# Kernel tuning notes

Measured on AMD Instinct MI355X. Metric: run time of the kernel, lower is better.

The kernel has to match this reference:

```python
import jax, jax.numpy as jnp
import numpy as np

B, S, D = 1, 2048, 2048
H, G, HD = 32, 8, 64        # n_heads, n_kv_groups, head_dim
GS = H // G                  # group_size
ROPE_BASE = 10000.0


def _rope_tables(seq_len, head_dim):
    inv_freq = 1.0 / (ROPE_BASE ** (jnp.arange(0, head_dim, 2, dtype=jnp.float32) / head_dim))
    angles = jnp.arange(seq_len, dtype=jnp.float32)[:, None] * inv_freq[None, :]  # [S, HD/2]
    angles = jnp.concatenate([angles, angles], axis=-1)                            # [S, HD]
    return jnp.cos(angles), jnp.sin(angles)


def setup_inputs() -> dict:
    key = jax.random.key(0)
    ks = jax.random.split(key, 5)
    x = jax.random.normal(ks[0], (B, S, D), dtype=jnp.float32)
    mask = jnp.triu(jnp.ones((S, S), dtype=bool), k=1)  # True = masked (causal)
    cos_vals, sin_vals = _rope_tables(S, HD)
    scale = 0.02
    Wq = jax.random.normal(ks[1], (H * HD, D), dtype=jnp.float32) * scale
    Wk = jax.random.normal(ks[2], (G * HD, D), dtype=jnp.float32) * scale
    Wv = jax.random.normal(ks[3], (G * HD, D), dtype=jnp.float32) * scale
    Wo = jax.random.normal(ks[4], (D, H * HD), dtype=jnp.float32) * scale
    return {"x": x, "mask": mask, "cos_vals": cos_vals, "sin_vals": sin_vals,
            "Wq": Wq, "Wk": Wk, "Wv": Wv, "Wo": Wo}


def _apply_rope(t, cos, sin):
    # t: [b, heads, S, HD]; cos/sin: [S, HD]
    half = t.shape[-1] // 2
    t1, t2 = t[..., :half], t[..., half:]
    rotated = jnp.concatenate([-t2, t1], axis=-1)
    return t * cos[None, None] + rotated * sin[None, None]


def reference(x, mask, cos_vals, sin_vals, Wq, Wk, Wv, Wo):
    b, s, _ = x.shape
    q = (x @ Wq.T).reshape(b, s, H, HD).transpose(0, 2, 1, 3)   # [b,H,S,HD]
    k = (x @ Wk.T).reshape(b, s, G, HD).transpose(0, 2, 1, 3)   # [b,G,S,HD]
    v = (x @ Wv.T).reshape(b, s, G, HD).transpose(0, 2, 1, 3)   # [b,G,S,HD]
    q = _apply_rope(q, cos_vals, sin_vals)
    k = _apply_rope(k, cos_vals, sin_vals)
    # Group-broadcast instead of repeat_interleave (same math)
    q = q.reshape(b, G, GS, s, HD)
    scores = jnp.einsum('bghqd,bgkd->bghqk', q, k)              # [b,G,GS,S,S]
    scores = jnp.where(mask[None, None, None], -jnp.inf, scores)
    weights = jax.nn.softmax(scores / np.sqrt(HD).astype(np.float32), axis=-1)
    out = jnp.einsum('bghqk,bgkd->bghqd', weights, v)           # [b,G,GS,S,HD]
    out = out.reshape(b, H, s, HD).transpose(0, 2, 1, 3).reshape(b, s, H * HD)
    return out @ Wo.T
```

## Files before the change

kernel.cpp:

```cpp
#include <hip/hip_runtime.h>
#include <cstddef>
#include <cstdint>

#define S 2048
#define Dm 2048
#define NH 32
#define NG 8
#define HD 64

typedef __attribute__((ext_vector_type(8))) short bf16x8;
typedef __attribute__((ext_vector_type(4))) short bf16x4;
typedef __attribute__((ext_vector_type(4))) float f32x4;

__device__ __forceinline__ float fast_exp2(float x) { return __builtin_amdgcn_exp2f(x); }

__device__ __forceinline__ unsigned short f2bf(float f) {
  unsigned int u = __builtin_bit_cast(unsigned int, f);
  u = (u + 0x7fffu + ((u >> 16) & 1u)) >> 16;
  return (unsigned short)u;
}
__device__ __forceinline__ unsigned int pk2bf(float lo, float hi) {
  unsigned int a = __builtin_bit_cast(unsigned int, lo) + 0x8000u;
  unsigned int b = __builtin_bit_cast(unsigned int, hi) + 0x8000u;
  return (a >> 16) | (b & 0xffff0000u);
}
__device__ __forceinline__ void gl_lds16(const unsigned short* g, unsigned short* l) {
  __builtin_amdgcn_global_load_lds(
      (const __attribute__((address_space(1))) unsigned int*)g,
      (__attribute__((address_space(3))) unsigned int*)l, 16, 0, 0);
}

#define QSC 0.1803368801111601f

__global__ __launch_bounds__(256) void cvt_all(const float* __restrict__ x,
                                               const float* __restrict__ Wq,
                                               const float* __restrict__ Wk,
                                               const float* __restrict__ Wv,
                                               const float* __restrict__ Wo,
                                               unsigned short* __restrict__ xb,
                                               unsigned short* __restrict__ Wcat,
                                               unsigned short* __restrict__ Wob) {
  int i = blockIdx.x * 256 + threadIdx.x;
  const float4* src;
  ushort4* dst;
  if (i < 1048576)      { src = (const float4*)x  + i;             dst = (ushort4*)xb + i; }
  else if (i < 2097152) { src = (const float4*)Wq + (i - 1048576); dst = (ushort4*)Wcat + (i - 1048576); }
  else if (i < 2359296) { src = (const float4*)Wk + (i - 2097152); dst = (ushort4*)Wcat + 1048576 + (i - 2097152); }
  else if (i < 2621440) { src = (const float4*)Wv + (i - 2359296); dst = (ushort4*)Wcat + 1310720 + (i - 2359296); }
  else                  { src = (const float4*)Wo + (i - 2621440); dst = (ushort4*)Wob + (i - 2621440); }
  float4 v = *src;
  ushort4 o;
  o.x = f2bf(v.x); o.y = f2bf(v.y); o.z = f2bf(v.z); o.w = f2bf(v.w);
  *dst = o;
}

__global__ __launch_bounds__(256) void gemm_bf16(const unsigned short* __restrict__ A,
                                                 const unsigned short* __restrict__ B,
                                                 float* __restrict__ Cf,
                                                 unsigned short* __restrict__ Cb,
                                                 unsigned short* __restrict__ VtOut,
                                                 const float* __restrict__ cosv,
                                                 const float* __restrict__ sinv,
                                                 int M, int N, int K) {
  __shared__ __align__(16) unsigned short As[64 * 64];
  __shared__ __align__(16) unsigned short Bs[128 * 64];
  const int tid = threadIdx.x;
  const int lane = tid & 63, wave = tid >> 6;
  const int row0 = blockIdx.y * 64, col0 = blockIdx.x * 128;
  const int wr = (wave >> 1) * 32, wc = (wave & 1) * 64;

  f32x4 acc[2][4];
#pragma unroll
  for (int i = 0; i < 2; i++)
#pragma unroll
    for (int j = 0; j < 4; j++) acc[i][j] = (f32x4){0.f, 0.f, 0.f, 0.f};

  const int arow0 = tid >> 3, aslot0 = ((tid & 7) ^ (arow0 & 7)) * 8;
  const int arow1 = (tid + 256) >> 3, aslot1 = (((tid + 256) & 7) ^ (arow1 & 7)) * 8;
  const int fr = lane & 15, q4 = lane >> 4;

  for (int k0 = 0; k0 < K; k0 += 64) {
    gl_lds16(&A[(size_t)(row0 + arow0) * K + k0 + aslot0], &As[tid * 8]);
    gl_lds16(&A[(size_t)(row0 + arow1) * K + k0 + aslot1], &As[(tid + 256) * 8]);
#pragma unroll
    for (int b = 0; b < 4; b++) {
      int p = tid + b * 256;
      int r = p >> 3, sl = ((p & 7) ^ (r & 7)) * 8;
      gl_lds16(&B[(size_t)(col0 + r) * K + k0 + sl], &Bs[p * 8]);
    }
    __syncthreads();
#pragma unroll
    for (int kk = 0; kk < 2; kk++) {
      bf16x8 af[2], bfr[4];
#pragma unroll
      for (int i = 0; i < 2; i++) {
        int R = wr + i * 16 + fr;
        af[i] = *(const bf16x8*)&As[R * 64 + ((q4 + kk * 4) ^ (R & 7)) * 8];
      }
#pragma unroll
      for (int j = 0; j < 4; j++) {
        int R = wc + j * 16 + fr;
        bfr[j] = *(const bf16x8*)&Bs[R * 64 + ((q4 + kk * 4) ^ (R & 7)) * 8];
      }
#pragma unroll
      for (int i = 0; i < 2; i++)
#pragma unroll
        for (int j = 0; j < 4; j++)
          acc[i][j] = __builtin_amdgcn_mfma_f32_16x16x32_bf16(af[i], bfr[j], acc[i][j], 0, 0, 0);
    }
    __syncthreads();
  }

  const int cc = lane & 15, cr = (lane >> 4) * 4;

  if (cosv) {
#pragma unroll
    for (int i = 0; i < 2; i++) {
      int grb = row0 + wr + i * 16 + cr;
#pragma unroll
      for (int j = 0; j < 2; j++) {
        int gc = col0 + wc + j * 16 + cc;
        if (gc < 2560) {
          int d = j * 16 + cc;
          float qs = (gc < 2048) ? QSC : 1.0f;
#pragma unroll
          for (int r = 0; r < 4; r++) {
            float c = cosv[(grb + r) * 64 + d];
            float s = sinv[(grb + r) * 64 + d];
            float t1 = acc[i][j][r], t2 = acc[i][j + 2][r];
            acc[i][j][r]     = (t1 * c - t2 * s) * qs;
            acc[i][j + 2][r] = (t2 * c + t1 * s) * qs;
          }
        }
      }
    }
  }

#pragma unroll
  for (int i = 0; i < 2; i++)
#pragma unroll
    for (int j = 0; j < 4; j++) {
      int gc = col0 + wc + j * 16 + cc;
#pragma unroll
      for (int r = 0; r < 4; r++) {
        int gr = row0 + wr + i * 16 + cr + r;
        if (cosv) {
          if (gc >= 2560) VtOut[(size_t)(gc - 2560) * 2048 + gr] = f2bf(acc[i][j][r]);
          else            Cb[(size_t)gr * N + gc] = f2bf(acc[i][j][r]);
        } else if (Cf)    Cf[(size_t)gr * N + gc] = acc[i][j][r];
        else              Cb[(size_t)gr * N + gc] = f2bf(acc[i][j][r]);
      }
    }
}

__global__ __launch_bounds__(256, 2) void flash_mfma(const unsigned short* __restrict__ QKV,
                                                     const unsigned short* __restrict__ Vt_g,
                                                     unsigned short* __restrict__ Ob) {
  __shared__ __align__(16) unsigned short Ks[2][64 * 64];
  __shared__ __align__(16) unsigned short Vs[2][64 * 64];

  const int tid = threadIdx.x;
  const int lane = tid & 63, wave = tid >> 6;
  const int m15 = lane & 15, q4 = lane >> 4;

  const int L = blockIdx.x;
  const int h = L & 31, g = h >> 2;
  const int u0 = L >> 5, a = u0 >> 3, b = u0 & 7;
  const int u = (a == 0) ? 15 - b : b;
  const int qb = u * 128;
  const int ntiles = 2 * u + 2;

  bf16x8 qf[2][2];
#pragma unroll
  for (int f = 0; f < 2; f++) {
    const size_t qrow = (size_t)(qb + f * 64 + wave * 16 + m15) * 3072 + h * 64;
    qf[f][0] = *(const bf16x8*)&QKV[qrow + q4 * 8];
    qf[f][1] = *(const bf16x8*)&QKV[qrow + 32 + q4 * 8];
  }

  f32x4 accO[2][4];
  float l_lane[2] = {0.f, 0.f};
#pragma unroll
  for (int f = 0; f < 2; f++)
#pragma unroll
    for (int v = 0; v < 4; v++) accO[f][v] = (f32x4){0.f, 0.f, 0.f, 0.f};

  const int p0 = wave * 128 + lane, p1 = p0 + 64;
  const int sr0 = p0 >> 3, so0 = ((p0 & 7) ^ (sr0 & 7)) * 8;
  const int sr1 = p1 >> 3, so1 = ((p1 & 7) ^ (sr1 & 7)) * 8;

#pragma unroll
  for (int t = 0; t < 2; t++) {
    const int k0 = t * 64;
    gl_lds16(&QKV[(size_t)(k0 + sr0) * 3072 + 2048 + g * 64 + so0], &Ks[t][p0 * 8]);
    gl_lds16(&QKV[(size_t)(k0 + sr1) * 3072 + 2048 + g * 64 + so1], &Ks[t][p1 * 8]);
    gl_lds16(&Vt_g[(size_t)(g * 64 + sr0) * 2048 + k0 + so0], &Vs[t][p0 * 8]);
    gl_lds16(&Vt_g[(size_t)(g * 64 + sr1) * 2048 + k0 + so1], &Vs[t][p1 * 8]);
  }

  for (int t = 0; t < ntiles; t++) {
    if (t + 1 < ntiles) asm volatile("s_waitcnt vmcnt(4)" ::: "memory");
    else                asm volatile("s_waitcnt vmcnt(0)" ::: "memory");
    asm volatile("s_barrier" ::: "memory");

    const unsigned short* Kb = Ks[t & 1];
    const unsigned short* Vb = Vs[t & 1];
    const bool act0 = (t < ntiles - 1);

    f32x4 sc[2][4];
#pragma unroll
    for (int kt = 0; kt < 4; kt++) {
      const int krow = kt * 16 + m15;
      bf16x8 kf0 = *(const bf16x8*)&Kb[krow * 64 + (q4 ^ (krow & 7)) * 8];
      bf16x8 kf1 = *(const bf16x8*)&Kb[krow * 64 + ((q4 + 4) ^ (krow & 7)) * 8];
      f32x4 z1 = (f32x4){0.f, 0.f, 0.f, 0.f};
      z1 = __builtin_amdgcn_mfma_f32_16x16x32_bf16(kf0, qf[1][0], z1, 0, 0, 0);
      sc[1][kt] = __builtin_amdgcn_mfma_f32_16x16x32_bf16(kf1, qf[1][1], z1, 0, 0, 0);
      if (act0) {
        f32x4 z0 = (f32x4){0.f, 0.f, 0.f, 0.f};
        z0 = __builtin_amdgcn_mfma_f32_16x16x32_bf16(kf0, qf[0][0], z0, 0, 0, 0);
        sc[0][kt] = __builtin_amdgcn_mfma_f32_16x16x32_bf16(kf1, qf[0][1], z0, 0, 0, 0);
      }
    }

    bf16x8 pA0[2], pA1[2];
#pragma unroll
    for (int f = 0; f < 2; f++) {
      if (f == 0 && !act0) continue;
      if (t == 2 * u + f) {
        const int qo = wave * 16 + m15;
#pragma unroll
        for (int kt = 0; kt < 4; kt++)
#pragma unroll
          for (int r = 0; r < 4; r++)
            if (kt * 16 + q4 * 4 + r > qo) sc[f][kt][r] = -1e30f;
      }
      float rs = 0.f;
#pragma unroll
      for (int kt = 0; kt < 4; kt++)
#pragma unroll
        for (int r = 0; r < 4; r++) {
          float p = fast_exp2(sc[f][kt][r]);
          sc[f][kt][r] = p;
          rs += p;
        }
      l_lane[f] += rs;

      int4 pa0, pa1;
      pa0.x = pk2bf(sc[f][0][0], sc[f][0][1]); pa0.y = pk2bf(sc[f][0][2], sc[f][0][3]);
      pa0.z = pk2bf(sc[f][1][0], sc[f][1][1]); pa0.w = pk2bf(sc[f][1][2], sc[f][1][3]);
      pa1.x = pk2bf(sc[f][2][0], sc[f][2][1]); pa1.y = pk2bf(sc[f][2][2], sc[f][2][3]);
      pa1.z = pk2bf(sc[f][3][0], sc[f][3][1]); pa1.w = pk2bf(sc[f][3][2], sc[f][3][3]);
      pA0[f] = __builtin_bit_cast(bf16x8, pa0);
      pA1[f] = __builtin_bit_cast(bf16x8, pa1);
    }

#pragma unroll
    for (int vt = 0; vt < 4; vt++) {
      const int vrow = vt * 16 + m15;
      const int base = vrow * 64, sw = vrow & 7, half = (q4 & 1) * 4, c1 = q4 >> 1;
      bf16x4 w00 = *(const bf16x4*)&Vb[base + (c1 ^ sw) * 8 + half];
      bf16x4 w01 = *(const bf16x4*)&Vb[base + ((c1 + 2) ^ sw) * 8 + half];
      bf16x4 w10 = *(const bf16x4*)&Vb[base + ((c1 + 4) ^ sw) * 8 + half];
      bf16x4 w11 = *(const bf16x4*)&Vb[base + ((c1 + 6) ^ sw) * 8 + half];
      bf16x8 vB0 = __builtin_shufflevector(w00, w01, 0, 1, 2, 3, 4, 5, 6, 7);
      bf16x8 vB1 = __builtin_shufflevector(w10, w11, 0, 1, 2, 3, 4, 5, 6, 7);
      accO[1][vt] = __builtin_amdgcn_mfma_f32_16x16x32_bf16(pA0[1], vB0, accO[1][vt], 0, 0, 0);
      accO[1][vt] = __builtin_amdgcn_mfma_f32_16x16x32_bf16(pA1[1], vB1, accO[1][vt], 0, 0, 0);
      if (act0) {
        accO[0][vt] = __builtin_amdgcn_mfma_f32_16x16x32_bf16(pA0[0], vB0, accO[0][vt], 0, 0, 0);
        accO[0][vt] = __builtin_amdgcn_mfma_f32_16x16x32_bf16(pA1[0], vB1, accO[0][vt], 0, 0, 0);
      }
    }

    asm volatile("s_barrier" ::: "memory");
    if (t + 2 < ntiles) {
      const int k2 = (t + 2) * 64;
      unsigned short* Kn = (unsigned short*)Ks[t & 1];
      unsigned short* Vn = (unsigned short*)Vs[t & 1];
      gl_lds16(&QKV[(size_t)(k2 + sr0) * 3072 + 2048 + g * 64 + so0], &Kn[p0 * 8]);
      gl_lds16(&QKV[(size_t)(k2 + sr1) * 3072 + 2048 + g * 64 + so1], &Kn[p1 * 8]);
      gl_lds16(&Vt_g[(size_t)(g * 64 + sr0) * 2048 + k2 + so0], &Vn[p0 * 8]);
      gl_lds16(&Vt_g[(size_t)(g * 64 + sr1) * 2048 + k2 + so1], &Vn[p1 * 8]);
    }
  }

#pragma unroll
  for (int f = 0; f < 2; f++) {
    float lsum = l_lane[f];
    lsum += __shfl_xor(lsum, 16);
    lsum += __shfl_xor(lsum, 32);
    float lr[4];
#pragma unroll
    for (int r = 0; r < 4; r++) lr[r] = 1.0f / __shfl(lsum, q4 * 20 + r);
#pragma unroll
    for (int vt = 0; vt < 4; vt++)
#pragma unroll
      for (int r = 0; r < 4; r++) {
        int row = qb + f * 64 + wave * 16 + q4 * 4 + r;
        Ob[(size_t)row * 2048 + h * 64 + vt * 16 + m15] = f2bf(accO[f][vt][r] * lr[r]);
      }
  }
}

extern "C" void kernel_launch(void* const* d_in, const int* in_sizes, int n_in,
                              void* d_out, int out_size, void* d_ws, size_t ws_size,
                              hipStream_t stream) {
  const float* x    = (const float*)d_in[0];
  const float* cosv = (const float*)d_in[2];
  const float* sinv = (const float*)d_in[3];
  const float* Wq   = (const float*)d_in[4];
  const float* Wk   = (const float*)d_in[5];
  const float* Wv   = (const float*)d_in[6];
  const float* Wo   = (const float*)d_in[7];
  float* out = (float*)d_out;

  unsigned short* xb   = (unsigned short*)d_ws;
  unsigned short* Wcat = xb + (size_t)2048 * 2048;
  unsigned short* Wob  = Wcat + (size_t)3072 * 2048;
  unsigned short* QKV  = Wob + (size_t)2048 * 2048;
  unsigned short* Vt_g = QKV + (size_t)3072 * 2048;

  dim3 blk(256);
  cvt_all<<<14336, blk, 0, stream>>>(x, Wq, Wk, Wv, Wo, xb, Wcat, Wob);
  gemm_bf16<<<dim3(24, 32), blk, 0, stream>>>(xb, Wcat, nullptr, QKV, Vt_g, cosv, sinv, 2048, 3072, 2048);
  flash_mfma<<<512, blk, 0, stream>>>(QKV, Vt_g, xb);
  gemm_bf16<<<dim3(16, 32), blk, 0, stream>>>(xb, Wob, out, nullptr, nullptr, nullptr, nullptr, 2048, 2048, 2048);
}
```

Before: 221.1 us.

## Triple-buffer GEMM LDS tiles with async prefetch two steps ahead

Replaces the single-buffered load/sync/compute loop in the bf16 GEMM with a three-stage LDS ring buffer. Global-to-LDS copies for tile t+2 are issued before computing tile t, with a partial vmcnt wait and a single barrier per iteration. This aims to hide global memory latency behind MFMA work and drop one barrier per step. The cost is triple the shared memory (72KB), which may reduce occupancy, and reliance on hand-written waitcnt counts being correct.

```diff
diff --git a/kernel.cpp b/kernel.cpp
--- a/kernel.cpp
+++ b/kernel.cpp
@@ -62,8 +62,8 @@
                                                  const float* __restrict__ cosv,
                                                  const float* __restrict__ sinv,
                                                  int M, int N, int K) {
-  __shared__ __align__(16) unsigned short As[64 * 64];
-  __shared__ __align__(16) unsigned short Bs[128 * 64];
+  __shared__ __align__(16) unsigned short As[3][64 * 64];
+  __shared__ __align__(16) unsigned short Bs[3][128 * 64];
   const int tid = threadIdx.x;
   const int lane = tid & 63, wave = tid >> 6;
   const int row0 = blockIdx.y * 64, col0 = blockIdx.x * 128;
@@ -79,28 +79,52 @@
   const int arow1 = (tid + 256) >> 3, aslot1 = (((tid + 256) & 7) ^ (arow1 & 7)) * 8;
   const int fr = lane & 15, q4 = lane >> 4;
 
-  for (int k0 = 0; k0 < K; k0 += 64) {
-    gl_lds16(&A[(size_t)(row0 + arow0) * K + k0 + aslot0], &As[tid * 8]);
-    gl_lds16(&A[(size_t)(row0 + arow1) * K + k0 + aslot1], &As[(tid + 256) * 8]);
-#pragma unroll
-    for (int b = 0; b < 4; b++) {
-      int p = tid + b * 256;
-      int r = p >> 3, sl = ((p & 7) ^ (r & 7)) * 8;
-      gl_lds16(&B[(size_t)(col0 + r) * K + k0 + sl], &Bs[p * 8]);
-    }
-    __syncthreads();
+  int brow[4], bslot[4];
+#pragma unroll
+  for (int b = 0; b < 4; b++) {
+    int p = tid + b * 256;
+    brow[b] = p >> 3;
+    bslot[b] = ((p & 7) ^ (brow[b] & 7)) * 8;
+  }
+
+  const int nk = K >> 6;
+
+  auto stage = [&](int k0, int buf) {
+    gl_lds16(&A[(size_t)(row0 + arow0) * K + k0 + aslot0], &As[buf][tid * 8]);
+    gl_lds16(&A[(size_t)(row0 + arow1) * K + k0 + aslot1], &As[buf][(tid + 256) * 8]);
+#pragma unroll
+    for (int b = 0; b < 4; b++)
+      gl_lds16(&B[(size_t)(col0 + brow[b]) * K + k0 + bslot[b]], &Bs[buf][(tid + b * 256) * 8]);
+  };
+
+  stage(0, 0);
+  stage(64, 1);
+
+  int cur = 0;
+  for (int t = 0; t < nk; ++t) {
+    if (t + 1 < nk) asm volatile("s_waitcnt vmcnt(6)" ::: "memory");
+    else            asm volatile("s_waitcnt vmcnt(0)" ::: "memory");
+    asm volatile("s_barrier" ::: "memory");
+
+    if (t + 2 < nk) {
+      int sb = cur + 2; if (sb >= 3) sb -= 3;
+      stage((t + 2) << 6, sb);
+    }
+
+    const unsigned short* Ab = As[cur];
+    const unsigned short* Bb = Bs[cur];
 #pragma unroll
     for (int kk = 0; kk < 2; kk++) {
       bf16x8 af[2], bfr[4];
 #pragma unroll
       for (int i = 0; i < 2; i++) {
         int R = wr + i * 16 + fr;
-        af[i] = *(const bf16x8*)&As[R * 64 + ((q4 + kk * 4) ^ (R & 7)) * 8];
+        af[i] = *(const bf16x8*)&Ab[R * 64 + ((q4 + kk * 4) ^ (R & 7)) * 8];
       }
 #pragma unroll
       for (int j = 0; j < 4; j++) {
         int R = wc + j * 16 + fr;
-        bfr[j] = *(const bf16x8*)&Bs[R * 64 + ((q4 + kk * 4) ^ (R & 7)) * 8];
+        bfr[j] = *(const bf16x8*)&Bb[R * 64 + ((q4 + kk * 4) ^ (R & 7)) * 8];
       }
 #pragma unroll
       for (int i = 0; i < 2; i++)
@@ -108,7 +132,8 @@
         for (int j = 0; j < 4; j++)
           acc[i][j] = __builtin_amdgcn_mfma_f32_16x16x32_bf16(af[i], bfr[j], acc[i][j], 0, 0, 0);
     }
-    __syncthreads();
+
+    cur = cur + 1; if (cur == 3) cur = 0;
   }
 
   const int cc = lane & 15, cr = (lane >> 4) * 4;
```

Measured after the change: 241.9 us. +9.4%, slower.

## Double-buffer B tiles, load A fragments directly to registers, remap GEMM block order

Applied to the files above, without the earlier changes.

The GEMM now double-buffers the B tile in LDS with manual vmcnt waits so global loads for the next k-step overlap MFMA compute. The A operand skips LDS and is loaded straight from global memory into registers one step ahead. Workgroup IDs are remapped in groups of eight for better L2 locality. The attention kernel's barrier before refilling K/V now waits for outstanding LDS reads first. Risks include hand-counted vmcnt values breaking if the load count changes, and uncoalesced or redundant global reads of A across the two column waves.

```diff
diff --git a/kernel.cpp b/kernel.cpp
--- a/kernel.cpp
+++ b/kernel.cpp
@@ -28,6 +28,11 @@
   __builtin_amdgcn_global_load_lds(
       (const __attribute__((address_space(1))) unsigned int*)g,
       (__attribute__((address_space(3))) unsigned int*)l, 16, 0, 0);
+}
+
+__device__ __forceinline__ void lds_drain_barrier() {
+  asm volatile("s_waitcnt lgkmcnt(0)" ::: "memory");
+  asm volatile("s_barrier" ::: "memory");
 }
 
 #define QSC 0.1803368801111601f
@@ -62,12 +67,17 @@
                                                  const float* __restrict__ cosv,
                                                  const float* __restrict__ sinv,
                                                  int M, int N, int K) {
-  __shared__ __align__(16) unsigned short As[64 * 64];
-  __shared__ __align__(16) unsigned short Bs[128 * 64];
+  __shared__ __align__(16) unsigned short Bs[2][128 * 64];
   const int tid = threadIdx.x;
   const int lane = tid & 63, wave = tid >> 6;
-  const int row0 = blockIdx.y * 64, col0 = blockIdx.x * 128;
+
+  const int nwg = gridDim.x * gridDim.y;
+  const int flat = blockIdx.y * gridDim.x + blockIdx.x;
+  const int nf = (flat & 7) * (nwg >> 3) + (flat >> 3);
+  const int bx = nf % gridDim.x, by = nf / gridDim.x;
+  const int row0 = by * 64, col0 = bx * 128;
   const int wr = (wave >> 1) * 32, wc = (wave & 1) * 64;
+  const int fr = lane & 15, q4 = lane >> 4;
 
   f32x4 acc[2][4];
 #pragma unroll
@@ -75,40 +85,65 @@
 #pragma unroll
     for (int j = 0; j < 4; j++) acc[i][j] = (f32x4){0.f, 0.f, 0.f, 0.f};
 
-  const int arow0 = tid >> 3, aslot0 = ((tid & 7) ^ (arow0 & 7)) * 8;
-  const int arow1 = (tid + 256) >> 3, aslot1 = (((tid + 256) & 7) ^ (arow1 & 7)) * 8;
-  const int fr = lane & 15, q4 = lane >> 4;
-
-  for (int k0 = 0; k0 < K; k0 += 64) {
-    gl_lds16(&A[(size_t)(row0 + arow0) * K + k0 + aslot0], &As[tid * 8]);
-    gl_lds16(&A[(size_t)(row0 + arow1) * K + k0 + aslot1], &As[(tid + 256) * 8]);
+  const unsigned short* Ar0 = A + (size_t)(row0 + wr + fr) * K;
+  const unsigned short* Ar1 = A + (size_t)(row0 + wr + 16 + fr) * K;
+
+  const int nk = K >> 6;
+
+  auto stageB = [&](int k0, int buf) {
 #pragma unroll
     for (int b = 0; b < 4; b++) {
       int p = tid + b * 256;
       int r = p >> 3, sl = ((p & 7) ^ (r & 7)) * 8;
-      gl_lds16(&B[(size_t)(col0 + r) * K + k0 + sl], &Bs[p * 8]);
-    }
-    __syncthreads();
+      gl_lds16(&B[(size_t)(col0 + r) * K + k0 + sl], &Bs[buf][p * 8]);
+    }
+  };
+  auto loadA = [&](int k0, bf16x8 (&af)[2][2]) {
 #pragma unroll
     for (int kk = 0; kk < 2; kk++) {
-      bf16x8 af[2], bfr[4];
-#pragma unroll
-      for (int i = 0; i < 2; i++) {
-        int R = wr + i * 16 + fr;
-        af[i] = *(const bf16x8*)&As[R * 64 + ((q4 + kk * 4) ^ (R & 7)) * 8];
-      }
+      af[0][kk] = *(const bf16x8*)&Ar0[k0 + (q4 + kk * 4) * 8];
+      af[1][kk] = *(const bf16x8*)&Ar1[k0 + (q4 + kk * 4) * 8];
+    }
+  };
+  auto compute = [&](const unsigned short* Bb, const bf16x8 (&af)[2][2]) {
+#pragma unroll
+    for (int kk = 0; kk < 2; kk++) {
+      bf16x8 bfr[4];
 #pragma unroll
       for (int j = 0; j < 4; j++) {
         int R = wc + j * 16 + fr;
-        bfr[j] = *(const bf16x8*)&Bs[R * 64 + ((q4 + kk * 4) ^ (R & 7)) * 8];
+        bfr[j] = *(const bf16x8*)&Bb[R * 64 + ((q4 + kk * 4) ^ (R & 7)) * 8];
       }
 #pragma unroll
       for (int i = 0; i < 2; i++)
 #pragma unroll
         for (int j = 0; j < 4; j++)
-          acc[i][j] = __builtin_amdgcn_mfma_f32_16x16x32_bf16(af[i], bfr[j], acc[i][j], 0, 0, 0);
-    }
-    __syncthreads();
+          acc[i][j] = __builtin_amdgcn_mfma_f32_16x16x32_bf16(af[i][kk], bfr[j], acc[i][j], 0, 0, 0);
+    }
+  };
+
+  bf16x8 afE[2][2], afO[2][2];
+
+  stageB(0, 0);
+  loadA(0, afE);
+  stageB(64, 1);
+
+  for (int t = 0; t < nk; t += 2) {
+    if (t + 1 < nk) asm volatile("s_waitcnt vmcnt(4)" ::: "memory");
+    else            asm volatile("s_waitcnt vmcnt(0)" ::: "memory");
+    asm volatile("s_barrier" ::: "memory");
+    if (t + 1 < nk) loadA((t + 1) << 6, afO);
+    compute(Bs[0], afE);
+    lds_drain_barrier();
+    if (t + 2 < nk) stageB((t + 2) << 6, 0);
+
+    if (t + 2 < nk) asm volatile("s_waitcnt vmcnt(4)" ::: "memory");
+    else            asm volatile("s_waitcnt vmcnt(0)" ::: "memory");
+    asm volatile("s_barrier" ::: "memory");
+    if (t + 2 < nk) loadA((t + 2) << 6, afE);
+    compute(Bs[1], afO);
+    lds_drain_barrier();
+    if (t + 3 < nk) stageB((t + 3) << 6, 1);
   }
 
   const int cc = lane & 15, cr = (lane >> 4) * 4;
@@ -273,7 +308,7 @@
       }
     }
 
-    asm volatile("s_barrier" ::: "memory");
+    lds_drain_barrier();
     if (t + 2 < ntiles) {
       const int k2 = (t + 2) * 64;
       unsigned short* Kn = (unsigned short*)Ks[t & 1];
```

Measured after the change: 264.1 us. 1.19x slower.
